# Performance work log

Hardware: AMD Instinct MI355X
Metric: run time of the kernel (lower is better)

The kernel has to match this reference:

```python
import jax, jax.numpy as jnp
import numpy as np

B, S, D, V = 2, 2048, 4096, 32000

def setup_inputs() -> dict:
    key = jax.random.key(0)
    k1, k2, k3 = jax.random.split(key, 3)
    hidden_states = jax.random.normal(k1, (B, S, D), dtype=jnp.float32)
    W = jax.random.normal(k2, (V, D), dtype=jnp.float32) * 0.02  # lm_head weight [vocab, hidden]
    label_ids = jax.random.randint(k3, (B, S), 0, V, dtype=jnp.int64)
    return {"hidden_states": hidden_states, "W": W, "label_ids": label_ids}

def reference(hidden_states, W, label_ids):
    # lm_head: Linear(D, V, bias=False) -> logits [B, S, V], cast to fp32
    logits = jnp.einsum('bsd,vd->bsv', hidden_states, W).astype(jnp.float32)
    # shift: predict token t+1 from position t
    shift_logits = logits[:, :-1, :].reshape(-1, V)          # [B*(S-1), V]
    shift_labels = label_ids[:, 1:].reshape(-1)              # [B*(S-1)]
    logp = jax.nn.log_softmax(shift_logits, axis=-1)
    nll = -jnp.take_along_axis(logp, shift_labels[:, None], axis=1)[:, 0]
    loss = jnp.mean(nll)  # CrossEntropyLoss default reduction='mean'
    return loss, logits
```

## Files before the change

### kernel.cpp

```cpp
#include <hip/hip_runtime.h>
#include <hip/hip_bf16.h>

#define M_ 4096
#define N_ 32000
#define K_ 4096
#define S_ 2048
#define SM1 2047
#define NROWS 4094
#define NT_ 64

typedef __bf16 bf16x8 __attribute__((ext_vector_type(8)));
typedef float f32x4 __attribute__((ext_vector_type(4)));

#define GLDS16(g, l)                                                         \
  __builtin_amdgcn_global_load_lds(                                          \
      (__attribute__((address_space(1))) const void*)(g),                    \
      (__attribute__((address_space(3))) void*)(l), 16, 0, 0)
#define BAR() __builtin_amdgcn_s_barrier()
#define PRIO1() __builtin_amdgcn_s_setprio(1)
#define PRIO0() __builtin_amdgcn_s_setprio(0)
#define VMCNT(n) asm volatile("s_waitcnt vmcnt(" #n ")" ::: "memory")

__global__ __launch_bounds__(256) void cvt_f32_to_bf16(
    const float* __restrict__ in, bf16x8* __restrict__ out, long n8) {
  long i0 = (long)blockIdx.x * blockDim.x + threadIdx.x;
  long stride = (long)gridDim.x * blockDim.x;
  for (long i = i0; i < n8; i += stride) {
    const float4* p = reinterpret_cast<const float4*>(in) + i * 2;
    float4 a = p[0];
    float4 b = p[1];
    bf16x8 v;
    v[0] = (__bf16)a.x; v[1] = (__bf16)a.y; v[2] = (__bf16)a.z; v[3] = (__bf16)a.w;
    v[4] = (__bf16)b.x; v[5] = (__bf16)b.y; v[6] = (__bf16)b.z; v[7] = (__bf16)b.w;
    out[i] = v;
  }
}

__global__ __launch_bounds__(512, 2) void gemm256(
    const __bf16* __restrict__ A, const __bf16* __restrict__ B,
    float* __restrict__ C) {
  __shared__ __align__(1024) unsigned char smem[2][65536];

  const int tid = threadIdx.x;
  const int bid = blockIdx.x;
  const int wg = (bid & 7) * 250 + (bid >> 3);
  const int nblk = wg >> 4;
  const int mblk = wg & 15;
  const int m0 = mblk * 256;
  const int n0 = nblk * 256;

  const int w = tid >> 6;
  const int lane = tid & 63;
  const int wm = w >> 2;
  const int wn = w & 3;
  const int rl = lane & 15;
  const int cl = lane >> 4;
  const int srow = tid >> 3;
  const int scc = tid & 7;

  f32x4 acc[8][4];
#pragma unroll
  for (int i = 0; i < 8; ++i)
#pragma unroll
    for (int j = 0; j < 4; ++j) acc[i][j] = (f32x4){0.f, 0.f, 0.f, 0.f};

  auto stA2 = [&](int nbuf, int kt, int q) {
#pragma unroll
    for (int j = 0; j < 2; ++j) {
      const int r0 = q * 64 + j * 128;
      const int row = r0 + srow;
      const int c = scc ^ (row & 7);
      GLDS16(A + (size_t)(m0 + row) * K_ + kt * 64 + c * 8,
             &smem[nbuf][r0 * 128 + tid * 16]);
    }
  };
  auto stB2 = [&](int nbuf, int kt, int q) {
#pragma unroll
    for (int j = 0; j < 2; ++j) {
      const int cg = j * 512 + tid;
      const int rl_ = cg >> 3;
      const int row = ((rl_ >> 5) << 6) + q * 32 + (rl_ & 31);
      const int cc = cg & 7;
      const int c = cc ^ (row & 7);
      GLDS16(B + (size_t)(n0 + row) * K_ + kt * 64 + c * 8,
             &smem[nbuf][32768 + row * 128 + cc * 16]);
    }
  };
  auto ld = [&](const unsigned char* base, int row, int c) -> bf16x8 {
    return *(const bf16x8*)(base + row * 128 + (((c ^ row) & 7) << 4));
  };

  stA2(0, 0, 0); stB2(0, 0, 0); stA2(0, 0, 1); stB2(0, 0, 1);
  VMCNT(4);
  BAR();

  bf16x8 al[4][2], ah[4][2], b0r[2][2], b1r[2][2];
#pragma unroll
  for (int jj = 0; jj < 2; ++jj)
#pragma unroll
    for (int ks = 0; ks < 2; ++ks)
      b0r[jj][ks] = ld(smem[0] + 32768, wn * 64 + jj * 16 + rl, ks * 4 + cl);
#pragma unroll
  for (int ii = 0; ii < 4; ++ii)
#pragma unroll
    for (int ks = 0; ks < 2; ++ks)
      al[ii][ks] = ld(smem[0], wm * 128 + ii * 16 + rl, ks * 4 + cl);

  for (int s = 0; s < NT_; ++s) {
    const int cur = s & 1;
    const int nxt = cur ^ 1;
    const unsigned char* bA = smem[cur];
    const unsigned char* bB = smem[cur] + 32768;
    const bool st = (s + 1 < NT_);

    if (st) stA2(nxt, s + 1, 0);
    PRIO1();
#pragma unroll
    for (int ii = 0; ii < 4; ++ii)
#pragma unroll
      for (int jj = 0; jj < 2; ++jj)
#pragma unroll
        for (int ks = 0; ks < 2; ++ks)
          acc[ii][jj] = __builtin_amdgcn_mfma_f32_16x16x32_bf16(
              al[ii][ks], b0r[jj][ks], acc[ii][jj], 0, 0, 0);
    PRIO0();
    if (st) { VMCNT(2); } else { VMCNT(0); }
    BAR();

    if (st) stB2(nxt, s + 1, 0);
#pragma unroll
    for (int jj = 0; jj < 2; ++jj)
#pragma unroll
      for (int ks = 0; ks < 2; ++ks)
        b1r[jj][ks] = ld(bB, wn * 64 + 32 + jj * 16 + rl, ks * 4 + cl);
#pragma unroll
    for (int ii = 0; ii < 4; ++ii)
#pragma unroll
      for (int ks = 0; ks < 2; ++ks)
        ah[ii][ks] = ld(bA, wm * 128 + 64 + ii * 16 + rl, ks * 4 + cl);
    PRIO1();
#pragma unroll
    for (int ii = 0; ii < 4; ++ii)
#pragma unroll
      for (int jj = 0; jj < 2; ++jj)
#pragma unroll
        for (int ks = 0; ks < 2; ++ks)
          acc[ii][2 + jj] = __builtin_amdgcn_mfma_f32_16x16x32_bf16(
              al[ii][ks], b1r[jj][ks], acc[ii][2 + jj], 0, 0, 0);
    PRIO0();
    BAR();

    if (st) stA2(nxt, s + 1, 1);
    PRIO1();
#pragma unroll
    for (int ii = 0; ii < 4; ++ii)
#pragma unroll
      for (int jj = 0; jj < 2; ++jj)
#pragma unroll
        for (int ks = 0; ks < 2; ++ks)
          acc[4 + ii][jj] = __builtin_amdgcn_mfma_f32_16x16x32_bf16(
              ah[ii][ks], b0r[jj][ks], acc[4 + ii][jj], 0, 0, 0);
    PRIO0();
    BAR();

    if (st) stB2(nxt, s + 1, 1);
    PRIO1();
#pragma unroll
    for (int ii = 0; ii < 4; ++ii)
#pragma unroll
      for (int jj = 0; jj < 2; ++jj)
#pragma unroll
        for (int ks = 0; ks < 2; ++ks)
          acc[4 + ii][2 + jj] = __builtin_amdgcn_mfma_f32_16x16x32_bf16(
              ah[ii][ks], b1r[jj][ks], acc[4 + ii][2 + jj], 0, 0, 0);
    PRIO0();
    if (st) VMCNT(4);
    BAR();
    if (st) {
      const unsigned char* nA = smem[nxt];
      const unsigned char* nB = smem[nxt] + 32768;
#pragma unroll
      for (int jj = 0; jj < 2; ++jj)
#pragma unroll
        for (int ks = 0; ks < 2; ++ks)
          b0r[jj][ks] = ld(nB, wn * 64 + jj * 16 + rl, ks * 4 + cl);
#pragma unroll
      for (int ii = 0; ii < 4; ++ii)
#pragma unroll
        for (int ks = 0; ks < 2; ++ks)
          al[ii][ks] = ld(nA, wm * 128 + ii * 16 + rl, ks * 4 + cl);
    }
  }

#pragma unroll
  for (int i = 0; i < 8; ++i)
#pragma unroll
    for (int j = 0; j < 4; ++j)
#pragma unroll
      for (int r = 0; r < 4; ++r) {
        const int grow = m0 + wm * 128 + i * 16 + cl * 4 + r;
        const int gcol = n0 + wn * 64 + j * 16 + rl;
        C[(size_t)grow * N_ + gcol] = acc[i][j][r];
      }
}

__global__ __launch_bounds__(256) void gemm_fb(const float* __restrict__ Ap,
                                               const float* __restrict__ Bp,
                                               float* __restrict__ Cp) {
  __shared__ __align__(1024) unsigned char smem[2][16384];
  const int tid = threadIdx.x;
  const int bid = blockIdx.x;
  const int swz = (bid & 7) * 1000 + (bid >> 3);
  const int nblk = swz >> 5;
  const int mblk = swz & 31;
  const int m0 = mblk * 128;
  const int n0 = nblk * 128;
  const int w = tid >> 6, lane = tid & 63;
  const int wm = w >> 1, wn = w & 1;
  const int rl = lane & 15, cl = lane >> 4;

  f32x4 acc[4][4];
#pragma unroll
  for (int i = 0; i < 4; ++i)
#pragma unroll
    for (int j = 0; j < 4; ++j) acc[i][j] = (f32x4){0.f, 0.f, 0.f, 0.f};

  auto stage = [&](int buf, int kt) {
    const int k0 = kt * 32;
#pragma unroll
    for (int j = 0; j < 2; ++j) {
      const int t = j * 256 + tid;
      const int row = t >> 2;
      const int c = t & 3;
      const int rp = row >> 1;
      const int pp = ((row & 1) * 4 + c) ^ (rp & 7);
      const int lb = rp * 128 + pp * 16;
      {
        const float4* g = (const float4*)(Ap + (size_t)(m0 + row) * K_ + k0 + c * 8);
        float4 x = g[0], y = g[1];
        bf16x8 v;
        v[0] = (__bf16)x.x; v[1] = (__bf16)x.y; v[2] = (__bf16)x.z; v[3] = (__bf16)x.w;
        v[4] = (__bf16)y.x; v[5] = (__bf16)y.y; v[6] = (__bf16)y.z; v[7] = (__bf16)y.w;
        *(bf16x8*)(&smem[buf][lb]) = v;
      }
      {
        const float4* g = (const float4*)(Bp + (size_t)(n0 + row) * K_ + k0 + c * 8);
        float4 x = g[0], y = g[1];
        bf16x8 v;
        v[0] = (__bf16)x.x; v[1] = (__bf16)x.y; v[2] = (__bf16)x.z; v[3] = (__bf16)x.w;
        v[4] = (__bf16)y.x; v[5] = (__bf16)y.y; v[6] = (__bf16)y.z; v[7] = (__bf16)y.w;
        *(bf16x8*)(&smem[buf][8192 + lb]) = v;
      }
    }
  };
  auto ldfrag = [&](const unsigned char* base, int row, int c) -> bf16x8 {
    const int rp = row >> 1;
    const int pp = ((row & 1) * 4 + c) ^ (rp & 7);
    return *(const bf16x8*)(base + rp * 128 + pp * 16);
  };
  auto compute = [&](int buf) {
    const unsigned char* bA = smem[buf];
    const unsigned char* bB = smem[buf] + 8192;
    bf16x8 af[4], bfv[4];
#pragma unroll
    for (int i = 0; i < 4; ++i) af[i] = ldfrag(bA, wm * 64 + i * 16 + rl, cl);
#pragma unroll
    for (int j = 0; j < 4; ++j) bfv[j] = ldfrag(bB, wn * 64 + j * 16 + rl, cl);
#pragma unroll
    for (int i = 0; i < 4; ++i)
#pragma unroll
      for (int j = 0; j < 4; ++j)
        acc[i][j] = __builtin_amdgcn_mfma_f32_16x16x32_bf16(af[i], bfv[j],
                                                            acc[i][j], 0, 0, 0);
  };

  stage(0, 0);
  __syncthreads();
  for (int kt = 0; kt < 128; kt += 2) {
    if (kt + 1 < 128) stage(1, kt + 1);
    compute(0);
    __syncthreads();
    if (kt + 2 < 128) stage(0, kt + 2);
    compute(1);
    __syncthreads();
  }
#pragma unroll
  for (int i = 0; i < 4; ++i)
#pragma unroll
    for (int j = 0; j < 4; ++j)
#pragma unroll
      for (int r = 0; r < 4; ++r) {
        const int grow = m0 + wm * 64 + i * 16 + cl * 4 + r;
        const int gcol = n0 + wn * 64 + j * 16 + rl;
        Cp[(size_t)grow * N_ + gcol] = acc[i][j][r];
      }
}

__global__ __launch_bounds__(256) void ce_rows(const float* __restrict__ logits,
                                               const int* __restrict__ labels,
                                               float* __restrict__ nll) {
  const int r = blockIdx.x;
  const int b = r / SM1;
  const int t = r - b * SM1;
  const float* row = logits + (size_t)(b * S_ + t) * N_;
  float m = -3.4e38f, s = 0.f;
  const float4* row4 = (const float4*)row;
  for (int i = threadIdx.x; i < 7936; i += 256) {
    float4 v = row4[i];
    float mx = fmaxf(fmaxf(v.x, v.y), fmaxf(v.z, v.w));
    if (mx > m) { s *= __expf(m - mx); m = mx; }
    s += __expf(v.x - m) + __expf(v.y - m) + __expf(v.z - m) + __expf(v.w - m);
  }
  {
    float v = row[31744 + threadIdx.x];
    if (v > m) { s *= __expf(m - v); m = v; }
    s += __expf(v - m);
  }
#pragma unroll
  for (int o = 32; o > 0; o >>= 1) {
    float m2 = __shfl_xor(m, o), s2 = __shfl_xor(s, o);
    float mn = fmaxf(m, m2);
    s = s * __expf(m - mn) + s2 * __expf(m2 - mn);
    m = mn;
  }
  __shared__ float rm[4], rs[4];
  if ((threadIdx.x & 63) == 0) { rm[threadIdx.x >> 6] = m; rs[threadIdx.x >> 6] = s; }
  __syncthreads();
  if (threadIdx.x == 0) {
    float M = fmaxf(fmaxf(rm[0], rm[1]), fmaxf(rm[2], rm[3]));
    float S = rs[0] * __expf(rm[0] - M) + rs[1] * __expf(rm[1] - M) +
              rs[2] * __expf(rm[2] - M) + rs[3] * __expf(rm[3] - M);
    nll[r] = M + __logf(S) - row[labels[b * S_ + t + 1]];
  }
}

__global__ __launch_bounds__(256) void reduce_loss(const float* __restrict__ nll,
                                                   float* __restrict__ out) {
  float s = 0.f;
  for (int i = threadIdx.x; i < NROWS; i += 256) s += nll[i];
#pragma unroll
  for (int o = 32; o > 0; o >>= 1) s += __shfl_xor(s, o);
  __shared__ float sb[4];
  if ((threadIdx.x & 63) == 0) sb[threadIdx.x >> 6] = s;
  __syncthreads();
  if (threadIdx.x == 0) out[0] = (sb[0] + sb[1] + sb[2] + sb[3]) / (float)NROWS;
}

extern "C" void kernel_launch(void* const* d_in, const int* in_sizes, int n_in,
                              void* d_out, int out_size, void* d_ws,
                              size_t ws_size, hipStream_t stream) {
  const float* h = (const float*)d_in[0];
  const float* Wf = (const float*)d_in[1];
  const int* labels = (const int*)d_in[2];
  float* out = (float*)d_out;
  float* logits = out + 1;

  const size_t abytes = (size_t)M_ * K_ * 2;
  const size_t bbytes = (size_t)N_ * K_ * 2;
  const size_t need = abytes + bbytes + (size_t)NROWS * sizeof(float);

  if (ws_size >= need) {
    unsigned char* base = (unsigned char*)d_ws;
    __bf16* hA = (__bf16*)base;
    __bf16* wB = (__bf16*)(base + abytes);
    float* nll = (float*)(base + abytes + bbytes);
    cvt_f32_to_bf16<<<2048, 256, 0, stream>>>(h, (bf16x8*)hA,
                                              (long)((size_t)M_ * K_ / 8));
    cvt_f32_to_bf16<<<4096, 256, 0, stream>>>(Wf, (bf16x8*)wB,
                                              (long)((size_t)N_ * K_ / 8));
    gemm256<<<2000, 512, 0, stream>>>(hA, wB, logits);
    ce_rows<<<4094, 256, 0, stream>>>(logits, labels, nll);
    reduce_loss<<<1, 256, 0, stream>>>(nll, out);
  } else {
    float* nll = (float*)d_ws;
    gemm_fb<<<8000, 256, 0, stream>>>(h, Wf, logits);
    ce_rows<<<4094, 256, 0, stream>>>(logits, labels, nll);
    reduce_loss<<<1, 256, 0, stream>>>(nll, out);
  }
}
```

Baseline: 1.244 ms.

## Fuse per-tile softmax partials into GEMM epilogue and deepen load pipeline

The GEMM epilogue now computes a per-row max and sum-of-exp for each 256-column tile and writes these partials to workspace. A small combine kernel merges them with online-softmax rescaling and subtracts the label logit. This replaces the separate cross-entropy pass that re-read the full 4096x32000 logits matrix. The main loop is also reordered to prefetch two K-steps ahead, issuing the next-next stage into the current buffer. The costs are extra epilogue reductions, barriers and workspace, plus a more delicate vmcnt accounting in the pipeline.

```diff
diff --git a/kernel.cpp b/kernel.cpp
--- a/kernel.cpp
+++ b/kernel.cpp
@@ -8,6 +8,7 @@
 #define SM1 2047
 #define NROWS 4094
 #define NT_ 64
+#define NB_ 125
 
 typedef __bf16 bf16x8 __attribute__((ext_vector_type(8)));
 typedef float f32x4 __attribute__((ext_vector_type(4)));
@@ -38,7 +39,7 @@
 
 __global__ __launch_bounds__(512, 2) void gemm256(
     const __bf16* __restrict__ A, const __bf16* __restrict__ B,
-    float* __restrict__ C) {
+    float* __restrict__ C, float* __restrict__ pm, float* __restrict__ ps) {
   __shared__ __align__(1024) unsigned char smem[2][65536];
 
   const int tid = threadIdx.x;
@@ -91,7 +92,8 @@
   };
 
   stA2(0, 0, 0); stB2(0, 0, 0); stA2(0, 0, 1); stB2(0, 0, 1);
-  VMCNT(4);
+  stA2(1, 1, 0); stB2(1, 1, 0);
+  VMCNT(8);
   BAR();
 
   bf16x8 al[4][2], ah[4][2], b0r[2][2], b1r[2][2];
@@ -113,7 +115,7 @@
     const unsigned char* bB = smem[cur] + 32768;
     const bool st = (s + 1 < NT_);
 
-    if (st) stA2(nxt, s + 1, 0);
+    if (st) stA2(nxt, s + 1, 1);
     PRIO1();
 #pragma unroll
     for (int ii = 0; ii < 4; ++ii)
@@ -124,10 +126,10 @@
           acc[ii][jj] = __builtin_amdgcn_mfma_f32_16x16x32_bf16(
               al[ii][ks], b0r[jj][ks], acc[ii][jj], 0, 0, 0);
     PRIO0();
-    if (st) { VMCNT(2); } else { VMCNT(0); }
-    BAR();
-
-    if (st) stB2(nxt, s + 1, 0);
+    if (st) { VMCNT(6); } else { VMCNT(0); }
+    BAR();
+
+    if (st) stB2(nxt, s + 1, 1);
 #pragma unroll
     for (int jj = 0; jj < 2; ++jj)
 #pragma unroll
@@ -150,7 +152,6 @@
     PRIO0();
     BAR();
 
-    if (st) stA2(nxt, s + 1, 1);
     PRIO1();
 #pragma unroll
     for (int ii = 0; ii < 4; ++ii)
@@ -161,9 +162,24 @@
           acc[4 + ii][jj] = __builtin_amdgcn_mfma_f32_16x16x32_bf16(
               ah[ii][ks], b0r[jj][ks], acc[4 + ii][jj], 0, 0, 0);
     PRIO0();
-    BAR();
-
-    if (st) stB2(nxt, s + 1, 1);
+    if (st) VMCNT(4);
+    BAR();
+
+    if (s + 2 < NT_) { stA2(cur, s + 2, 0); stB2(cur, s + 2, 0); }
+    if (st) {
+      const unsigned char* nA = smem[nxt];
+      const unsigned char* nB = smem[nxt] + 32768;
+#pragma unroll
+      for (int jj = 0; jj < 2; ++jj)
+#pragma unroll
+        for (int ks = 0; ks < 2; ++ks)
+          b0r[jj][ks] = ld(nB, wn * 64 + jj * 16 + rl, ks * 4 + cl);
+#pragma unroll
+      for (int ii = 0; ii < 4; ++ii)
+#pragma unroll
+        for (int ks = 0; ks < 2; ++ks)
+          al[ii][ks] = ld(nA, wm * 128 + ii * 16 + rl, ks * 4 + cl);
+    }
     PRIO1();
 #pragma unroll
     for (int ii = 0; ii < 4; ++ii)
@@ -174,22 +190,7 @@
           acc[4 + ii][2 + jj] = __builtin_amdgcn_mfma_f32_16x16x32_bf16(
               ah[ii][ks], b1r[jj][ks], acc[4 + ii][2 + jj], 0, 0, 0);
     PRIO0();
-    if (st) VMCNT(4);
-    BAR();
-    if (st) {
-      const unsigned char* nA = smem[nxt];
-      const unsigned char* nB = smem[nxt] + 32768;
-#pragma unroll
-      for (int jj = 0; jj < 2; ++jj)
-#pragma unroll
-        for (int ks = 0; ks < 2; ++ks)
-          b0r[jj][ks] = ld(nB, wn * 64 + jj * 16 + rl, ks * 4 + cl);
-#pragma unroll
-      for (int ii = 0; ii < 4; ++ii)
-#pragma unroll
-        for (int ks = 0; ks < 2; ++ks)
-          al[ii][ks] = ld(nA, wm * 128 + ii * 16 + rl, ks * 4 + cl);
-    }
+    BAR();
   }
 
 #pragma unroll
@@ -202,6 +203,78 @@
         const int gcol = n0 + wn * 64 + j * 16 + rl;
         C[(size_t)grow * N_ + gcol] = acc[i][j][r];
       }
+
+  float* red = (float*)smem;
+  float* red2 = (float*)(smem[0] + 4096);
+  float fmx[8][4];
+  {
+    BAR();
+#pragma unroll
+    for (int i = 0; i < 8; ++i)
+#pragma unroll
+      for (int r = 0; r < 4; ++r) {
+        float v = fmaxf(fmaxf(acc[i][0][r], acc[i][1][r]),
+                        fmaxf(acc[i][2][r], acc[i][3][r]));
+#pragma unroll
+        for (int o = 1; o < 16; o <<= 1) v = fmaxf(v, __shfl_xor(v, o));
+        if (rl == 0) red[wn * 256 + wm * 128 + i * 16 + cl * 4 + r] = v;
+      }
+    BAR();
+#pragma unroll
+    for (int i = 0; i < 8; ++i)
+#pragma unroll
+      for (int r = 0; r < 4; ++r) {
+        const int row = wm * 128 + i * 16 + cl * 4 + r;
+        fmx[i][r] = fmaxf(fmaxf(red[row], red[256 + row]),
+                          fmaxf(red[512 + row], red[768 + row]));
+        float sv = __expf(acc[i][0][r] - fmx[i][r]) +
+                   __expf(acc[i][1][r] - fmx[i][r]) +
+                   __expf(acc[i][2][r] - fmx[i][r]) +
+                   __expf(acc[i][3][r] - fmx[i][r]);
+#pragma unroll
+        for (int o = 1; o < 16; o <<= 1) sv += __shfl_xor(sv, o);
+        if (rl == 0) red2[wn * 256 + row] = sv;
+      }
+    BAR();
+    if (tid < 256) {
+      const int row = tid;
+      const float Mv = fmaxf(fmaxf(red[row], red[256 + row]),
+                             fmaxf(red[512 + row], red[768 + row]));
+      const float Sv = red2[row] + red2[256 + row] + red2[512 + row] +
+                       red2[768 + row];
+      pm[(size_t)(m0 + row) * NB_ + nblk] = Mv;
+      ps[(size_t)(m0 + row) * NB_ + nblk] = Sv;
+    }
+  }
+}
+
+__global__ __launch_bounds__(64) void ce_combine(
+    const float* __restrict__ pm, const float* __restrict__ ps,
+    const float* __restrict__ logits, const int* __restrict__ labels,
+    float* __restrict__ nll) {
+  const int r = blockIdx.x;
+  const int b = r / SM1;
+  const int t = r - b * SM1;
+  const int m = b * S_ + t;
+  const int lane = threadIdx.x;
+  float M = -3.4e38f, Ssum = 0.f;
+  for (int j = lane; j < NB_; j += 64) {
+    const float mj = pm[(size_t)m * NB_ + j];
+    const float sj = ps[(size_t)m * NB_ + j];
+    if (mj > M) { Ssum *= __expf(M - mj); M = mj; }
+    Ssum += sj * __expf(mj - M);
+  }
+#pragma unroll
+  for (int o = 32; o > 0; o >>= 1) {
+    const float M2 = __shfl_xor(M, o), S2 = __shfl_xor(Ssum, o);
+    const float mn = fmaxf(M, M2);
+    Ssum = Ssum * __expf(M - mn) + S2 * __expf(M2 - mn);
+    M = mn;
+  }
+  if (lane == 0) {
+    const int lbl = labels[b * S_ + t + 1];
+    nll[r] = M + __logf(Ssum) - logits[(size_t)m * N_ + lbl];
+  }
 }
 
 __global__ __launch_bounds__(256) void gemm_fb(const float* __restrict__ Ap,
@@ -357,19 +430,22 @@
 
   const size_t abytes = (size_t)M_ * K_ * 2;
   const size_t bbytes = (size_t)N_ * K_ * 2;
-  const size_t need = abytes + bbytes + (size_t)NROWS * sizeof(float);
+  const size_t pbytes = (size_t)M_ * NB_ * 4;
+  const size_t need = abytes + bbytes + 2 * pbytes + (size_t)NROWS * 4;
 
   if (ws_size >= need) {
     unsigned char* base = (unsigned char*)d_ws;
     __bf16* hA = (__bf16*)base;
     __bf16* wB = (__bf16*)(base + abytes);
-    float* nll = (float*)(base + abytes + bbytes);
+    float* pm = (float*)(base + abytes + bbytes);
+    float* psum = (float*)(base + abytes + bbytes + pbytes);
+    float* nll = (float*)(base + abytes + bbytes + 2 * pbytes);
     cvt_f32_to_bf16<<<2048, 256, 0, stream>>>(h, (bf16x8*)hA,
                                               (long)((size_t)M_ * K_ / 8));
     cvt_f32_to_bf16<<<4096, 256, 0, stream>>>(Wf, (bf16x8*)wB,
                                               (long)((size_t)N_ * K_ / 8));
-    gemm256<<<2000, 512, 0, stream>>>(hA, wB, logits);
-    ce_rows<<<4094, 256, 0, stream>>>(logits, labels, nll);
+    gemm256<<<2000, 512, 0, stream>>>(hA, wB, logits, pm, psum);
+    ce_combine<<<NROWS, 64, 0, stream>>>(pm, psum, logits, labels, nll);
     reduce_loss<<<1, 256, 0, stream>>>(nll, out);
   } else {
     float* nll = (float*)d_ws;
```

Result: faster. 1.198 ms (-3.7%).
